# Optimization experiments

Measured on AMD Instinct MI355X. Metric: run time of the kernel, lower is better.

Reference implementation:

```python
import jax, jax.numpy as jnp
import numpy as np

# pywt db4 analysis filters (dec_lo, dec_hi), length 8
DEC_LO = np.array([-0.010597401784997278, 0.032883011666982945, 0.030841381835986965,
                   -0.18703481171888114, -0.02798376941698385, 0.6308807679295904,
                   0.7148465705525415, 0.23037781330885523], dtype=np.float32)
DEC_HI = np.array([-0.23037781330885523, 0.7148465705525415, -0.6308807679295904,
                   -0.02798376941698385, 0.18703481171888114, 0.030841381835986965,
                   -0.032883011666982945, -0.010597401784997278], dtype=np.float32)


def setup_inputs() -> dict:
    key = jax.random.key(0)
    x = jax.random.normal(key, (32, 3, 512, 512), dtype=jnp.float32)
    dec = jnp.stack([jnp.asarray(DEC_LO), jnp.asarray(DEC_HI)])  # (2, 8)
    return {"x": x, "dec": dec}


def _afb1d_last(x, dec):
    """Analysis filter bank along last axis: circular pad (end), stride-2
    cross-correlation with lo/hi filters. x: (..., L) -> (lo, hi) each (..., L//2)."""
    L = x.shape[-1]
    taps = dec.shape[-1]
    pad = taps - 1
    xp = jnp.concatenate([x, x[..., :pad]], axis=-1)          # circular pad at end
    flat = xp.reshape(-1, 1, xp.shape[-1])                    # (N, 1, L+pad)
    out = jax.lax.conv_general_dilated(
        flat, dec[:, None, :], window_strides=(2,), padding='VALID',
        dimension_numbers=('NCH', 'OIH', 'NCH'))              # (N, 2, L//2)
    out = out.reshape(*x.shape[:-1], 2, L // 2)
    return out[..., 0, :], out[..., 1, :]


def reference(x, dec):
    B, C, H, W = x.shape
    xr = x.reshape(B * C, H, W)
    # row pass (along W)
    lo_w, hi_w = _afb1d_last(xr, dec)                         # (BC, H, W//2)
    # column pass (along H): move H to last axis
    lo_t = jnp.swapaxes(lo_w, -2, -1)                         # (BC, W//2, H)
    hi_t = jnp.swapaxes(hi_w, -2, -1)
    ll, lh = _afb1d_last(lo_t, dec)                           # (BC, W//2, H//2)
    hl, hh = _afb1d_last(hi_t, dec)
    coeffs = jnp.stack([ll, lh, hl, hh], axis=1)              # (BC, 4, W//2, H//2)
    coeffs = jnp.swapaxes(coeffs, -2, -1)                     # (BC, 4, H//2, W//2)
    return coeffs.reshape(B, C * 4, H // 2, W // 2)
```

## Files before the change

### kernel.cpp

```cpp
#include <hip/hip_runtime.h>


#define TI 16
#define TJ 64
#define PR (2*TI + 6)
#define PC (2*TJ + 6)
#define HH 512
#define WW 512

__global__ __launch_bounds__(256)
void dwt2d_db4_kernel(const float* __restrict__ x,
                      const float* __restrict__ dec,
                      float* __restrict__ out) {
    __shared__ float sm_x[PR][PC];
    __shared__ float sm_lo[PR][TJ];
    __shared__ float sm_hi[PR][TJ];

    const int tid = threadIdx.x;
    const int jt  = blockIdx.x;
    const int it  = blockIdx.y;
    const int bc  = blockIdx.z;

    const int rowBase = it * (2 * TI);
    const int colBase = jt * (2 * TJ);

    float flo[8], fhi[8];
#pragma unroll
    for (int k = 0; k < 8; ++k) { flo[k] = dec[k]; fhi[k] = dec[8 + k]; }

    const float* xb = x + (size_t)bc * HH * WW;

    for (int idx = tid; idx < PR * PC; idx += 256) {
        int r = idx / PC;
        int c = idx - r * PC;
        int gr = rowBase + r; if (gr >= HH) gr -= HH;
        int gc = colBase + c; if (gc >= WW) gc -= WW;
        sm_x[r][c] = xb[gr * WW + gc];
    }
    __syncthreads();

    for (int idx = tid; idx < PR * TJ; idx += 256) {
        int r = idx >> 6;
        int j = idx & 63;
        float lo = 0.f, hi = 0.f;
#pragma unroll
        for (int q = 0; q < 8; ++q) {
            float v = sm_x[r][2 * j + q];
            lo += v * flo[q];
            hi += v * fhi[q];
        }
        sm_lo[r][j] = lo;
        sm_hi[r][j] = hi;
    }
    __syncthreads();

    for (int idx = tid; idx < TI * TJ; idx += 256) {
        int i = idx >> 6;
        int j = idx & 63;
        float ll = 0.f, lh = 0.f, hl = 0.f, hh = 0.f;
#pragma unroll
        for (int p = 0; p < 8; ++p) {
            float a = sm_lo[2 * i + p][j];
            float b = sm_hi[2 * i + p][j];
            ll += a * flo[p];
            lh += a * fhi[p];
            hl += b * flo[p];
            hh += b * fhi[p];
        }
        int oi = it * TI + i;
        int oj = jt * TJ + j;
        size_t base = ((size_t)(bc * 4) * 256 + oi) * 256 + oj;
        out[base]               = ll;
        out[base + 1 * 65536]   = lh;
        out[base + 2 * 65536]   = hl;
        out[base + 3 * 65536]   = hh;
    }
}

extern "C" void kernel_launch(void* const* d_in, const int* in_sizes, int n_in,
                              void* d_out, int out_size, void* d_ws, size_t ws_size,
                              hipStream_t stream) {
    const float* x   = (const float*)d_in[0];
    const float* dec = (const float*)d_in[1];
    float* out = (float*)d_out;

    dim3 grid(256 / TJ, 256 / TI, 96);
    dim3 block(256);
    dwt2d_db4_kernel<<<grid, block, 0, stream>>>(x, dec, out);
}
```

Measured before the change: 192.0 us.

## Vectorize DWT loads, shared-memory passes and output stores with float4

Global loads into shared memory now use float4 with a scalar fallback for the circular wrap, and the row width is padded to 136 for alignment. The row pass has each thread compute two adjacent outputs from three float4 shared reads. The column pass has each thread produce four columns at once. Outputs are written as 16-byte nontemporal stores. The aim is fewer memory instructions and better global bandwidth on a memory-bound kernel, at the cost of more registers per thread and possible LDS bank conflicts on the strided float4 reads.

```diff
diff --git a/kernel.cpp b/kernel.cpp
--- a/kernel.cpp
+++ b/kernel.cpp
@@ -4,17 +4,19 @@
 #define TI 16
 #define TJ 64
 #define PR (2*TI + 6)
-#define PC (2*TJ + 6)
+#define PC 136
 #define HH 512
 #define WW 512
+
+typedef float v4f __attribute__((ext_vector_type(4)));
 
 __global__ __launch_bounds__(256)
 void dwt2d_db4_kernel(const float* __restrict__ x,
                       const float* __restrict__ dec,
                       float* __restrict__ out) {
-    __shared__ float sm_x[PR][PC];
-    __shared__ float sm_lo[PR][TJ];
-    __shared__ float sm_hi[PR][TJ];
+    __shared__ __align__(16) float sm_x[PR][PC];
+    __shared__ __align__(16) float sm_lo[PR][TJ];
+    __shared__ __align__(16) float sm_hi[PR][TJ];
 
     const int tid = threadIdx.x;
     const int jt  = blockIdx.x;
@@ -30,50 +32,78 @@
 
     const float* xb = x + (size_t)bc * HH * WW;
 
-    for (int idx = tid; idx < PR * PC; idx += 256) {
-        int r = idx / PC;
-        int c = idx - r * PC;
-        int gr = rowBase + r; if (gr >= HH) gr -= HH;
-        int gc = colBase + c; if (gc >= WW) gc -= WW;
-        sm_x[r][c] = xb[gr * WW + gc];
+    {
+        const int C4 = PC / 4;
+        for (int idx = tid; idx < PR * C4; idx += 256) {
+            int r  = idx / C4;
+            int c4 = idx - r * C4;
+            int gr = rowBase + r; if (gr >= HH) gr -= HH;
+            int gc = colBase + 4 * c4;
+            const float* src = xb + gr * WW;
+            float4 v;
+            if (gc + 3 < WW) {
+                v = *(const float4*)(src + gc);
+            } else {
+                v = make_float4(src[gc & (WW-1)], src[(gc+1) & (WW-1)],
+                                src[(gc+2) & (WW-1)], src[(gc+3) & (WW-1)]);
+            }
+            *(float4*)&sm_x[r][4 * c4] = v;
+        }
     }
     __syncthreads();
 
-    for (int idx = tid; idx < PR * TJ; idx += 256) {
-        int r = idx >> 6;
-        int j = idx & 63;
-        float lo = 0.f, hi = 0.f;
+    for (int task = tid; task < PR * (TJ / 2); task += 256) {
+        int r = task >> 5;
+        int t = task & 31;
+        const float* xr = &sm_x[r][4 * t];
+        float4 v0 = *(const float4*)(xr);
+        float4 v1 = *(const float4*)(xr + 4);
+        float4 v2 = *(const float4*)(xr + 8);
+        float w[12] = { v0.x, v0.y, v0.z, v0.w,
+                        v1.x, v1.y, v1.z, v1.w,
+                        v2.x, v2.y, v2.z, v2.w };
+        float lo0 = 0.f, hi0 = 0.f, lo1 = 0.f, hi1 = 0.f;
 #pragma unroll
         for (int q = 0; q < 8; ++q) {
-            float v = sm_x[r][2 * j + q];
-            lo += v * flo[q];
-            hi += v * fhi[q];
+            lo0 += w[q]     * flo[q];
+            hi0 += w[q]     * fhi[q];
+            lo1 += w[q + 2] * flo[q];
+            hi1 += w[q + 2] * fhi[q];
         }
-        sm_lo[r][j] = lo;
-        sm_hi[r][j] = hi;
+        *(float2*)&sm_lo[r][2 * t] = make_float2(lo0, lo1);
+        *(float2*)&sm_hi[r][2 * t] = make_float2(hi0, hi1);
     }
     __syncthreads();
 
-    for (int idx = tid; idx < TI * TJ; idx += 256) {
-        int i = idx >> 6;
-        int j = idx & 63;
-        float ll = 0.f, lh = 0.f, hl = 0.f, hh = 0.f;
+    {
+        int i  = tid >> 4;
+        int jb = tid & 15;
+        int j0 = 4 * jb;
+        float llx=0.f, lly=0.f, llz=0.f, llw=0.f;
+        float lhx=0.f, lhy=0.f, lhz=0.f, lhw=0.f;
+        float hlx=0.f, hly=0.f, hlz=0.f, hlw=0.f;
+        float hhx=0.f, hhy=0.f, hhz=0.f, hhw=0.f;
 #pragma unroll
         for (int p = 0; p < 8; ++p) {
-            float a = sm_lo[2 * i + p][j];
-            float b = sm_hi[2 * i + p][j];
-            ll += a * flo[p];
-            lh += a * fhi[p];
-            hl += b * flo[p];
-            hh += b * fhi[p];
+            float4 a = *(const float4*)&sm_lo[2 * i + p][j0];
+            float4 b = *(const float4*)&sm_hi[2 * i + p][j0];
+            float cl = flo[p], ch = fhi[p];
+            llx += a.x * cl; lly += a.y * cl; llz += a.z * cl; llw += a.w * cl;
+            lhx += a.x * ch; lhy += a.y * ch; lhz += a.z * ch; lhw += a.w * ch;
+            hlx += b.x * cl; hly += b.y * cl; hlz += b.z * cl; hlw += b.w * cl;
+            hhx += b.x * ch; hhy += b.y * ch; hhz += b.z * ch; hhw += b.w * ch;
         }
         int oi = it * TI + i;
-        int oj = jt * TJ + j;
+        int oj = jt * TJ + j0;
         size_t base = ((size_t)(bc * 4) * 256 + oi) * 256 + oj;
-        out[base]               = ll;
-        out[base + 1 * 65536]   = lh;
-        out[base + 2 * 65536]   = hl;
-        out[base + 3 * 65536]   = hh;
+        v4f ll = { llx, lly, llz, llw };
+        v4f lh = { lhx, lhy, lhz, lhw };
+        v4f hl = { hlx, hly, hlz, hlw };
+        v4f hh = { hhx, hhy, hhz, hhw };
+        __builtin_nontemporal_store(ll, (v4f*)&out[base]);
+        __builtin_nontemporal_store(lh, (v4f*)&out[base + 1 * 65536]);
+        __builtin_nontemporal_store(hl, (v4f*)&out[base + 2 * 65536]);
+        __builtin_nontemporal_store(hh, (v4f*)&out[base + 3 * 65536]);
     }
 }
 
```

Result: faster. 180.3 us (-6.1%).
